# Kernel tuning notes

Hardware: AMD Instinct MI355X
Metric: run time of the kernel (lower is better)

Reference implementation:

```python
import jax, jax.numpy as jnp
import numpy as np

T = 800_000      # total words across all sentences
S = 2048         # total sentences
B = 32           # number of sequences (documents)
M = 64           # max sentences per sequence (here exactly 64 each)
D_IN = 256
D_OUT = 128


def setup_inputs() -> dict:
    key = jax.random.key(0)
    k_tok, k_w, k_b = jax.random.split(key, 3)
    rng = np.random.default_rng(0)

    # ragged word counts per sentence, each >= 1, summing to T
    lengths = rng.multinomial(T - S, np.full(S, 1.0 / S)) + 1
    seg_ids = jnp.asarray(np.repeat(np.arange(S, dtype=np.int32), lengths))

    # sentence -> (document, position-in-document)
    sent_batch = jnp.asarray(np.repeat(np.arange(B, dtype=np.int32), M))
    sent_pos = jnp.asarray(np.tile(np.arange(M, dtype=np.int32), B))

    tokens = jax.random.normal(k_tok, (T, D_IN), dtype=jnp.float32)
    # nn.Linear default init scale ~ 1/sqrt(in_features)
    bound = 1.0 / np.sqrt(D_IN)
    weight = jax.random.uniform(k_w, (D_OUT, D_IN), jnp.float32, -bound, bound)
    bias = jax.random.uniform(k_b, (D_OUT,), jnp.float32, -bound, bound)
    return {"tokens": tokens, "weight": weight, "bias": bias,
            "seg_ids": seg_ids, "sent_batch": sent_batch, "sent_pos": sent_pos}


def reference(tokens, weight, bias, seg_ids, sent_batch, sent_pos):
    # per-word linear: [T, D_OUT]
    h = tokens @ weight.T + bias
    # max-pool words within each sentence: [S, D_OUT]
    sent = jax.ops.segment_max(h, seg_ids, num_segments=S)
    # pad_sequence(batch_first=True) -> zero-padded [B, M, D_OUT]
    out = jnp.zeros((B, M, D_OUT), dtype=h.dtype).at[sent_batch, sent_pos].set(sent)
    return out
```

## Files before the change

### kernel.cpp

```cpp
#include <hip/hip_runtime.h>
#include <hip/hip_bf16.h>

#define T_WORDS 800000
#define S_SENT 2048
#define DIN 256
#define DOUT 128
#define CHUNK 32

typedef short bf16x8 __attribute__((ext_vector_type(8)));
typedef float f32x4 __attribute__((ext_vector_type(4)));

union V16 { bf16x8 v; unsigned int u[4]; };

__device__ __forceinline__ unsigned int pk2(float lo, float hi) {
  __hip_bfloat162 h = __float22bfloat162_rn(float2{lo, hi});
  unsigned int u;
  __builtin_memcpy(&u, &h, sizeof(u));
  return u;
}

__device__ __forceinline__ unsigned short f2bf(float f) {
  unsigned int u = __builtin_bit_cast(unsigned int, f);
  u += 0x7fffu + ((u >> 16) & 1u);
  return (unsigned short)(u >> 16);
}

__global__ void prep_kernel(const float* __restrict__ weight,
                            const int* __restrict__ seg,
                            unsigned short* __restrict__ wsB,
                            int* __restrict__ starts) {
  int tid = blockIdx.x * blockDim.x + threadIdx.x;
  int stride = gridDim.x * blockDim.x;
  for (int j = tid; j < DOUT * DIN; j += stride)
    wsB[j] = f2bf(weight[j]);
  for (int j = tid; j < T_WORDS; j += stride) {
    if (j == 0) {
      starts[seg[0]] = 0;
    } else {
      int s1 = seg[j], s0 = seg[j - 1];
      if (s1 != s0) starts[s1] = j;
    }
  }
}

__global__ __launch_bounds__(256, 3) void pool_kernel(
    const float* __restrict__ tokens,
    const float* __restrict__ bias,
    const unsigned short* __restrict__ wsB,
    const int* __restrict__ starts,
    const int* __restrict__ sent_batch,
    const int* __restrict__ sent_pos,
    float* __restrict__ out) {
  __shared__ alignas(16) unsigned short Alds[2][CHUNK * DIN];

  const int s = blockIdx.x;
  const int start = starts[s];
  const int end = (s == S_SENT - 1) ? T_WORDS : starts[s + 1];
  const int lane = (int)(threadIdx.x & 63);
  const int wv = (int)(threadIdx.x >> 6);

  bf16x8 bfrag[2][8];
#pragma unroll
  for (int n = 0; n < 2; ++n) {
    const int col = 32 * wv + 16 * n + (lane & 15);
    const unsigned short* wrow = wsB + col * DIN + 8 * (lane >> 4);
#pragma unroll
    for (int kk = 0; kk < 8; ++kk)
      bfrag[n][kk] = *(const bf16x8*)(wrow + 32 * kk);
  }

  const int srow0 = (int)(threadIdx.x >> 5);
  const int sk8 = (int)(threadIdx.x & 31);

  float runmax0 = -INFINITY, runmax1 = -INFINITY;
  float4 pf[4][2];

#define ISSUE(WBASE)                                                          \
  {                                                                           \
    _Pragma("unroll") for (int it = 0; it < 4; ++it) {                        \
      int word = (WBASE) + srow0 + 8 * it;                                    \
      if (word < end) {                                                       \
        const float4* src =                                                   \
            (const float4*)(tokens + (size_t)word * DIN + sk8 * 8);           \
        pf[it][0] = src[0];                                                   \
        pf[it][1] = src[1];                                                   \
      }                                                                       \
    }                                                                         \
  }

#define WRITE(WBASE, BUF)                                                     \
  {                                                                           \
    _Pragma("unroll") for (int it = 0; it < 4; ++it) {                        \
      int row = srow0 + 8 * it;                                               \
      bool valid = (WBASE) + row < end;                                       \
      V16 w;                                                                  \
      w.u[0] = valid ? pk2(pf[it][0].x, pf[it][0].y) : 0xFF80FF80u;           \
      w.u[1] = valid ? pk2(pf[it][0].z, pf[it][0].w) : 0xFF80FF80u;           \
      w.u[2] = valid ? pk2(pf[it][1].x, pf[it][1].y) : 0xFF80FF80u;           \
      w.u[3] = valid ? pk2(pf[it][1].z, pf[it][1].w) : 0xFF80FF80u;           \
      int idx = (row * DIN + sk8 * 8) ^ ((row & 7) << 3);                     \
      *(bf16x8*)&Alds[BUF][idx] = w.v;                                        \
    }                                                                         \
  }

#define COMPUTE(BUF)                                                          \
  {                                                                           \
    _Pragma("unroll") for (int m = 0; m < 2; ++m) {                           \
      f32x4 acc0 = (f32x4){0.f, 0.f, 0.f, 0.f};                               \
      f32x4 acc1 = (f32x4){0.f, 0.f, 0.f, 0.f};                               \
      const int arow = 16 * m + (lane & 15);                                  \
      const int abase = arow * DIN + 8 * (lane >> 4);                         \
      const int axor = (lane & 7) << 3;                                       \
      _Pragma("unroll") for (int kk = 0; kk < 8; ++kk) {                      \
        bf16x8 a = *(const bf16x8*)&Alds[BUF][(abase + 32 * kk) ^ axor];      \
        acc0 = __builtin_amdgcn_mfma_f32_16x16x32_bf16(a, bfrag[0][kk], acc0, \
                                                       0, 0, 0);              \
        acc1 = __builtin_amdgcn_mfma_f32_16x16x32_bf16(a, bfrag[1][kk], acc1, \
                                                       0, 0, 0);              \
      }                                                                       \
      runmax0 = fmaxf(runmax0, fmaxf(fmaxf(acc0[0], acc0[1]),                 \
                                     fmaxf(acc0[2], acc0[3])));               \
      runmax1 = fmaxf(runmax1, fmaxf(fmaxf(acc1[0], acc1[1]),                 \
                                     fmaxf(acc1[2], acc1[3])));               \
    }                                                                         \
  }

#define BAR()                                                                 \
  {                                                                           \
    asm volatile("s_waitcnt lgkmcnt(0)" ::: "memory");                        \
    __builtin_amdgcn_s_barrier();                                             \
  }

  const int nch = (end - start + CHUNK - 1) / CHUNK;

  ISSUE(start)
  WRITE(start, 0)
  if (nch > 1) ISSUE(start + CHUNK)
  BAR()

  int c = 0;
  while (true) {
    int wb = start + c * CHUNK;
    if (c + 1 < nch) WRITE(wb + CHUNK, 1)
    if (c + 2 < nch) ISSUE(wb + 2 * CHUNK)
    COMPUTE(0)
    BAR()
    if (++c >= nch) break;

    wb = start + c * CHUNK;
    if (c + 1 < nch) WRITE(wb + CHUNK, 0)
    if (c + 2 < nch) ISSUE(wb + 2 * CHUNK)
    COMPUTE(1)
    BAR()
    if (++c >= nch) break;
  }

  runmax0 = fmaxf(runmax0, __shfl_xor(runmax0, 16, 64));
  runmax0 = fmaxf(runmax0, __shfl_xor(runmax0, 32, 64));
  runmax1 = fmaxf(runmax1, __shfl_xor(runmax1, 16, 64));
  runmax1 = fmaxf(runmax1, __shfl_xor(runmax1, 32, 64));

  if (lane < 16) {
    const int sb = sent_batch[s], sp = sent_pos[s];
    float* o = out + ((size_t)sb * 64 + sp) * DOUT;
    const int c0 = 32 * wv + lane;
    o[c0] = runmax0 + bias[c0];
    o[c0 + 16] = runmax1 + bias[c0 + 16];
  }
}

extern "C" void kernel_launch(void* const* d_in, const int* in_sizes, int n_in,
                              void* d_out, int out_size, void* d_ws, size_t ws_size,
                              hipStream_t stream) {
  const float* tokens = (const float*)d_in[0];
  const float* weight = (const float*)d_in[1];
  const float* bias   = (const float*)d_in[2];
  const int* seg      = (const int*)d_in[3];
  const int* sbatch   = (const int*)d_in[4];
  const int* spos     = (const int*)d_in[5];
  float* out = (float*)d_out;

  unsigned short* wsB = (unsigned short*)d_ws;
  int* starts = (int*)((char*)d_ws + DOUT * DIN * sizeof(unsigned short));

  prep_kernel<<<512, 256, 0, stream>>>(weight, seg, wsB, starts);
  pool_kernel<<<S_SENT, 256, 0, stream>>>(tokens, bias, wsB, starts, sbatch, spos, out);
}
```

Baseline: 160.8 us.

## Use persistent blocks that each process a word-balanced range of sentences

The pool kernel now launches a fixed grid of 768 blocks. Each block binary-searches the sentence start table to find the sentences whose starts fall in its equal share of the word range, then loops over those sentences, so the word load per block is more even and the grid fits a single wave. The prefetch depth drops from two chunks ahead to one: the global loads are issued before the MFMA compute and written to LDS after it. Each new sentence restarts the pipeline with an exposed load, which adds fill latency per sentence and may hide global latency less well.

```diff
diff --git a/kernel.cpp b/kernel.cpp
--- a/kernel.cpp
+++ b/kernel.cpp
@@ -6,6 +6,7 @@
 #define DIN 256
 #define DOUT 128
 #define CHUNK 32
+#define GRID_P 768
 
 typedef short bf16x8 __attribute__((ext_vector_type(8)));
 typedef float f32x4 __attribute__((ext_vector_type(4)));
@@ -36,11 +37,21 @@
   for (int j = tid; j < T_WORDS; j += stride) {
     if (j == 0) {
       starts[seg[0]] = 0;
+      starts[S_SENT] = T_WORDS;
     } else {
       int s1 = seg[j], s0 = seg[j - 1];
       if (s1 != s0) starts[s1] = j;
     }
   }
+}
+
+__device__ __forceinline__ int lbound(const int* __restrict__ a, int n, int v) {
+  int lo = 0, hi = n;
+  while (lo < hi) {
+    int m = (lo + hi) >> 1;
+    if (a[m] < v) lo = m + 1; else hi = m;
+  }
+  return lo;
 }
 
 __global__ __launch_bounds__(256, 3) void pool_kernel(
@@ -53,9 +64,12 @@
     float* __restrict__ out) {
   __shared__ alignas(16) unsigned short Alds[2][CHUNK * DIN];
 
-  const int s = blockIdx.x;
-  const int start = starts[s];
-  const int end = (s == S_SENT - 1) ? T_WORDS : starts[s + 1];
+  const int b = blockIdx.x;
+  const int tgt0 = (int)(((long long)b * T_WORDS + GRID_P - 1) / GRID_P);
+  const int tgt1 = (int)(((long long)(b + 1) * T_WORDS + GRID_P - 1) / GRID_P);
+  const int slo = lbound(starts, S_SENT, tgt0);
+  const int shi = lbound(starts, S_SENT, tgt1);
+
   const int lane = (int)(threadIdx.x & 63);
   const int wv = (int)(threadIdx.x >> 6);
 
@@ -72,14 +86,13 @@
   const int srow0 = (int)(threadIdx.x >> 5);
   const int sk8 = (int)(threadIdx.x & 31);
 
-  float runmax0 = -INFINITY, runmax1 = -INFINITY;
   float4 pf[4][2];
 
-#define ISSUE(WBASE)                                                          \
+#define ISSUE(WBASE, END)                                                     \
   {                                                                           \
     _Pragma("unroll") for (int it = 0; it < 4; ++it) {                        \
       int word = (WBASE) + srow0 + 8 * it;                                    \
-      if (word < end) {                                                       \
+      if (word < (END)) {                                                     \
         const float4* src =                                                   \
             (const float4*)(tokens + (size_t)word * DIN + sk8 * 8);           \
         pf[it][0] = src[0];                                                   \
@@ -88,11 +101,11 @@
     }                                                                         \
   }
 
-#define WRITE(WBASE, BUF)                                                     \
+#define WRITE(WBASE, END, BUF)                                                \
   {                                                                           \
     _Pragma("unroll") for (int it = 0; it < 4; ++it) {                        \
       int row = srow0 + 8 * it;                                               \
-      bool valid = (WBASE) + row < end;                                       \
+      bool valid = (WBASE) + row < (END);                                     \
       V16 w;                                                                  \
       w.u[0] = valid ? pk2(pf[it][0].x, pf[it][0].y) : 0xFF80FF80u;           \
       w.u[1] = valid ? pk2(pf[it][0].z, pf[it][0].w) : 0xFF80FF80u;           \
@@ -131,41 +144,46 @@
     __builtin_amdgcn_s_barrier();                                             \
   }
 
-  const int nch = (end - start + CHUNK - 1) / CHUNK;
-
-  ISSUE(start)
-  WRITE(start, 0)
-  if (nch > 1) ISSUE(start + CHUNK)
-  BAR()
-
-  int c = 0;
-  while (true) {
-    int wb = start + c * CHUNK;
-    if (c + 1 < nch) WRITE(wb + CHUNK, 1)
-    if (c + 2 < nch) ISSUE(wb + 2 * CHUNK)
-    COMPUTE(0)
+  for (int s = slo; s < shi; ++s) {
+    const int start = starts[s];
+    const int end = starts[s + 1];
+    const int nch = (end - start + CHUNK - 1) / CHUNK;
+
+    float runmax0 = -INFINITY, runmax1 = -INFINITY;
+
+    ISSUE(start, end)
+    WRITE(start, end, 0)
     BAR()
-    if (++c >= nch) break;
-
-    wb = start + c * CHUNK;
-    if (c + 1 < nch) WRITE(wb + CHUNK, 0)
-    if (c + 2 < nch) ISSUE(wb + 2 * CHUNK)
-    COMPUTE(1)
-    BAR()
-    if (++c >= nch) break;
-  }
-
-  runmax0 = fmaxf(runmax0, __shfl_xor(runmax0, 16, 64));
-  runmax0 = fmaxf(runmax0, __shfl_xor(runmax0, 32, 64));
-  runmax1 = fmaxf(runmax1, __shfl_xor(runmax1, 16, 64));
-  runmax1 = fmaxf(runmax1, __shfl_xor(runmax1, 32, 64));
-
-  if (lane < 16) {
-    const int sb = sent_batch[s], sp = sent_pos[s];
-    float* o = out + ((size_t)sb * 64 + sp) * DOUT;
-    const int c0 = 32 * wv + lane;
-    o[c0] = runmax0 + bias[c0];
-    o[c0 + 16] = runmax1 + bias[c0 + 16];
+
+    int c = 0;
+    while (true) {
+      int wb = start + c * CHUNK;
+      if (c + 1 < nch) ISSUE(wb + CHUNK, end)
+      COMPUTE(0)
+      if (c + 1 < nch) WRITE(wb + CHUNK, end, 1)
+      BAR()
+      if (++c >= nch) break;
+
+      wb = start + c * CHUNK;
+      if (c + 1 < nch) ISSUE(wb + CHUNK, end)
+      COMPUTE(1)
+      if (c + 1 < nch) WRITE(wb + CHUNK, end, 0)
+      BAR()
+      if (++c >= nch) break;
+    }
+
+    runmax0 = fmaxf(runmax0, __shfl_xor(runmax0, 16, 64));
+    runmax0 = fmaxf(runmax0, __shfl_xor(runmax0, 32, 64));
+    runmax1 = fmaxf(runmax1, __shfl_xor(runmax1, 16, 64));
+    runmax1 = fmaxf(runmax1, __shfl_xor(runmax1, 32, 64));
+
+    if (lane < 16) {
+      const int sb = sent_batch[s], sp = sent_pos[s];
+      float* o = out + ((size_t)sb * 64 + sp) * DOUT;
+      const int c0 = 32 * wv + lane;
+      o[c0] = runmax0 + bias[c0];
+      o[c0 + 16] = runmax1 + bias[c0 + 16];
+    }
   }
 }
 
@@ -184,5 +202,5 @@
   int* starts = (int*)((char*)d_ws + DOUT * DIN * sizeof(unsigned short));
 
   prep_kernel<<<512, 256, 0, stream>>>(weight, seg, wsB, starts);
-  pool_kernel<<<S_SENT, 256, 0, stream>>>(tokens, bias, wsB, starts, sbatch, spos, out);
-}
+  pool_kernel<<<GRID_P, 256, 0, stream>>>(tokens, bias, wsB, starts, sbatch, spos, out);
+}
```

Result: no change. 163.5 us (+1.7%).
